# Performance work log

Measured on AMD Instinct MI355X. Metric: run time of the kernel, lower is better.

Reference implementation:

```python
import jax, jax.numpy as jnp
import numpy as np

INPUT_DIM = 512
EMBED_DIM = 512
N_HEAD = 8
HEAD_DIM = EMBED_DIM // N_HEAD


def setup_inputs() -> dict:
    key = jax.random.key(0)
    k0, k1, k2 = jax.random.split(key, 3)
    B, S = 2, 4096
    X = jax.random.normal(k0, (B, S, INPUT_DIM), dtype=jnp.float32)
    # xavier_uniform for Linear weights (torch weight shape [out, in])
    def xavier(k, out_f, in_f):
        bound = float(np.sqrt(6.0 / (in_f + out_f)))
        return jax.random.uniform(k, (out_f, in_f), jnp.float32, -bound, bound)
    W_qkv = xavier(k1, 3 * EMBED_DIM, INPUT_DIM)
    b_qkv = jnp.zeros((3 * EMBED_DIM,), jnp.float32)
    W_o = xavier(k2, EMBED_DIM, EMBED_DIM)
    b_o = jnp.zeros((EMBED_DIM,), jnp.float32)
    return {"X": X, "W_qkv": W_qkv, "b_qkv": b_qkv, "W_o": W_o, "b_o": b_o}


def reference(X, W_qkv, b_qkv, W_o, b_o):
    B, S, _ = X.shape
    # fused QKV projection: [B,S,3E]
    qkv = jnp.einsum("bsd,ed->bse", X, W_qkv) + b_qkv
    # [B,S,H,3*hd] -> [B,H,S,3*hd]
    qkv = qkv.reshape(B, S, N_HEAD, 3 * HEAD_DIM).transpose(0, 2, 1, 3)
    q, k, v = jnp.split(qkv, 3, axis=-1)
    scale = 1.0 / jnp.sqrt(jnp.asarray(HEAD_DIM, q.dtype))
    logits = jnp.einsum("bhqd,bhkd->bhqk", q, k) * scale  # [B,H,S,S]
    attn = jax.nn.softmax(logits, axis=-1)
    vals = jnp.einsum("bhqk,bhkd->bhqd", attn, v)
    vals = vals.transpose(0, 2, 1, 3).reshape(B, S, EMBED_DIM)
    out = jnp.einsum("bse,fe->bsf", vals, W_o) + b_o
    return out
```

## Files before the change

### kernel.cpp

```cpp
#include <hip/hip_runtime.h>

#define S_   4096
#define D_IN 512
#define E_   512
#define HD   64

typedef __attribute__((ext_vector_type(8))) short short8;
typedef __attribute__((ext_vector_type(16))) float f32x16;

#define MFMA32(a, b, c) __builtin_amdgcn_mfma_f32_32x32x16_bf16((a), (b), (c), 0, 0, 0)

__device__ __forceinline__ unsigned short f2bf(float f) {
  unsigned u = __builtin_bit_cast(unsigned, f);
  u = (u + 0x7FFFu + ((u >> 16) & 1u)) >> 16;
  return (unsigned short)u;
}

__device__ __forceinline__ unsigned cvt_pk_bf16(float lo, float hi) {
  unsigned r;
  asm("v_cvt_pk_bf16_f32 %0, %1, %2" : "=v"(r) : "v"(lo), "v"(hi));
  return r;
}

__device__ __forceinline__ f32x16 splat16(float x) {
  f32x16 v;
#pragma unroll
  for (int i = 0; i < 16; ++i) v[i] = x;
  return v;
}

__global__ __launch_bounds__(256) void cvt3(const float* __restrict__ X,
                                            const float* __restrict__ Wq,
                                            const float* __restrict__ Wo,
                                            unsigned short* __restrict__ Xb,
                                            unsigned short* __restrict__ Wqb,
                                            unsigned short* __restrict__ Wob) {
  int bid = blockIdx.x;
  const float* src;
  unsigned short* dst;
  int i;
  if (bid < 4096)      { src = X;  dst = Xb;  i = bid * 256 + threadIdx.x; }
  else if (bid < 4864) { src = Wq; dst = Wqb; i = (bid - 4096) * 256 + threadIdx.x; }
  else                 { src = Wo; dst = Wob; i = (bid - 4864) * 256 + threadIdx.x; }
  float4 v = reinterpret_cast<const float4*>(src)[i];
  ushort4 o;
  o.x = f2bf(v.x); o.y = f2bf(v.y); o.z = f2bf(v.z); o.w = f2bf(v.w);
  reinterpret_cast<ushort4*>(dst)[i] = o;
}

__global__ __launch_bounds__(256, 3) void qkv_proj(const unsigned short* __restrict__ Xb,
                                                   const unsigned short* __restrict__ Wb,
                                                   const float* __restrict__ bias,
                                                   unsigned short* __restrict__ Qb,
                                                   unsigned short* __restrict__ Kb,
                                                   unsigned short* __restrict__ Vt) {
  __shared__ unsigned short Al[128][72];
  __shared__ unsigned short Bl[128][72];
  const int tid = threadIdx.x;
  const int w = tid >> 6, l = tid & 63, h = l >> 5, r31 = l & 31;
  const int wm = w >> 1, wn = w & 1;
  const int m0 = blockIdx.x * 128, n0 = blockIdx.y * 128;
  const int sr = tid >> 1, sc = tid & 1;

  f32x16 a00 = {}, a01 = {}, a10 = {}, a11 = {};
  const unsigned short* ap = Xb + (size_t)(m0 + sr) * D_IN + sc * 32;
  const unsigned short* bp = Wb + (size_t)(n0 + sr) * D_IN + sc * 32;
  for (int k0 = 0; k0 < D_IN; k0 += 64) {
    int4 av0 = *reinterpret_cast<const int4*>(ap + k0);
    int4 av1 = *reinterpret_cast<const int4*>(ap + k0 + 8);
    int4 av2 = *reinterpret_cast<const int4*>(ap + k0 + 16);
    int4 av3 = *reinterpret_cast<const int4*>(ap + k0 + 24);
    int4 bv0 = *reinterpret_cast<const int4*>(bp + k0);
    int4 bv1 = *reinterpret_cast<const int4*>(bp + k0 + 8);
    int4 bv2 = *reinterpret_cast<const int4*>(bp + k0 + 16);
    int4 bv3 = *reinterpret_cast<const int4*>(bp + k0 + 24);
    __syncthreads();
    *reinterpret_cast<int4*>(&Al[sr][sc * 32])      = av0;
    *reinterpret_cast<int4*>(&Al[sr][sc * 32 + 8])  = av1;
    *reinterpret_cast<int4*>(&Al[sr][sc * 32 + 16]) = av2;
    *reinterpret_cast<int4*>(&Al[sr][sc * 32 + 24]) = av3;
    *reinterpret_cast<int4*>(&Bl[sr][sc * 32])      = bv0;
    *reinterpret_cast<int4*>(&Bl[sr][sc * 32 + 8])  = bv1;
    *reinterpret_cast<int4*>(&Bl[sr][sc * 32 + 16]) = bv2;
    *reinterpret_cast<int4*>(&Bl[sr][sc * 32 + 24]) = bv3;
    __syncthreads();
#pragma unroll
    for (int c = 0; c < 4; ++c) {
      short8 aA = *reinterpret_cast<const short8*>(&Al[wm * 64 + r31][c * 16 + h * 8]);
      short8 aB = *reinterpret_cast<const short8*>(&Al[wm * 64 + 32 + r31][c * 16 + h * 8]);
      short8 bA = *reinterpret_cast<const short8*>(&Bl[wn * 64 + r31][c * 16 + h * 8]);
      short8 bB = *reinterpret_cast<const short8*>(&Bl[wn * 64 + 32 + r31][c * 16 + h * 8]);
      a00 = MFMA32(aA, bA, a00);
      a01 = MFMA32(aA, bB, a01);
      a10 = MFMA32(aB, bA, a10);
      a11 = MFMA32(aB, bB, a11);
    }
  }
#pragma unroll
  for (int rb = 0; rb < 2; ++rb)
#pragma unroll
    for (int cb = 0; cb < 2; ++cb) {
      const f32x16 A = rb ? (cb ? a11 : a10) : (cb ? a01 : a00);
      int n = n0 + wn * 64 + cb * 32 + r31;
      int hh = n / 192;
      int j = n - hh * 192;
      int t3 = j >> 6;
      int d = j & 63;
      float bn = bias[n];
      int mbase0 = m0 + wm * 64 + rb * 32 + h * 4;
#pragma unroll
      for (int rq = 0; rq < 4; ++rq) {
        int mb = mbase0 + rq * 8;
        int bb = mb >> 12;
        int ssb = mb & 4095;
        int bhh = bb * 8 + hh;
        if (t3 == 0) {
#pragma unroll
          for (int i = 0; i < 4; ++i)
            Qb[((size_t)bhh * S_ + ssb + i) * HD + d] =
                f2bf((A[rq * 4 + i] + bn) * (0.125f * 1.44269504088896f));
        } else if (t3 == 1) {
#pragma unroll
          for (int i = 0; i < 4; ++i)
            Kb[((size_t)bhh * S_ + ssb + i) * HD + d] = f2bf(A[rq * 4 + i] + bn);
        } else {
          int sp = (ssb & ~12) | ((ssb & 8) >> 1) | ((ssb & 4) << 1);
          ushort4 o;
          o.x = f2bf(A[rq * 4 + 0] + bn);
          o.y = f2bf(A[rq * 4 + 1] + bn);
          o.z = f2bf(A[rq * 4 + 2] + bn);
          o.w = f2bf(A[rq * 4 + 3] + bn);
          *reinterpret_cast<ushort4*>(&Vt[((size_t)bhh * HD + d) * S_ + sp]) = o;
        }
      }
    }
}

__global__ __launch_bounds__(512, 4) void attn_fwd(const unsigned short* __restrict__ Qb,
                                                   const unsigned short* __restrict__ Kb,
                                                   const unsigned short* __restrict__ Vt,
                                                   unsigned short* __restrict__ vals) {
  __shared__ char smem[73728];
  const int tid = threadIdx.x;
  const int w = tid >> 6, l = tid & 63, h = l >> 5, r31 = l & 31;
  const int grp = w >> 2;
  const int wq = w & 3;
  const int bh = blockIdx.x >> 5;
  const int q0 = (blockIdx.x & 31) * 128;
  const int lt256 = tid & 255;
  const int sr = lt256 >> 2, sc = lt256 & 3;

  unsigned short (*Kl)[64][72] =
      reinterpret_cast<unsigned short(*)[64][72]>(smem + grp * 36864);
  unsigned short (*Vl)[64][72] =
      reinterpret_cast<unsigned short(*)[64][72]>(smem + grp * 36864 + 18432);

  const int qrow = q0 + wq * 32 + r31;
  const unsigned short* qp = Qb + ((size_t)bh * S_ + qrow) * HD + h * 8;
  short8 bq[4];
#pragma unroll
  for (int c = 0; c < 4; ++c)
    bq[c] = *reinterpret_cast<const short8*>(qp + c * 16);

  f32x16 po0 = {}, po1 = {};
  float lacc = 0.f;

  const int kvbase = grp * 2048;
  const unsigned short* kptr = Kb + ((size_t)bh * S_ + kvbase + sr) * HD + sc * 16;
  const unsigned short* vptr = Vt + ((size_t)bh * HD + sr) * S_ + kvbase + sc * 16;

  {
    int4 kA = *reinterpret_cast<const int4*>(kptr);
    int4 kB = *reinterpret_cast<const int4*>(kptr + 8);
    int4 vA = *reinterpret_cast<const int4*>(vptr);
    int4 vB = *reinterpret_cast<const int4*>(vptr + 8);
    *reinterpret_cast<int4*>(&Kl[0][sr][sc * 16])     = kA;
    *reinterpret_cast<int4*>(&Kl[0][sr][sc * 16 + 8]) = kB;
    *reinterpret_cast<int4*>(&Vl[0][sr][sc * 16])     = vA;
    *reinterpret_cast<int4*>(&Vl[0][sr][sc * 16 + 8]) = vB;
  }
  __syncthreads();

  for (int kt = 0; kt < 32; ++kt) {
    const int cur = kt & 1;
    int4 kA, kB, vA, vB;
    if (kt < 31) {
      const unsigned short* kp = kptr + (size_t)(kt + 1) * 64 * HD;
      const unsigned short* vp = vptr + (kt + 1) * 64;
      kA = *reinterpret_cast<const int4*>(kp);
      kB = *reinterpret_cast<const int4*>(kp + 8);
      vA = *reinterpret_cast<const int4*>(vp);
      vB = *reinterpret_cast<const int4*>(vp + 8);
    }

    f32x16 s0 = splat16(-16.f), s1 = splat16(-16.f);
#pragma unroll
    for (int c = 0; c < 4; ++c) {
      short8 k0 = *reinterpret_cast<const short8*>(&Kl[cur][r31][c * 16 + h * 8]);
      s0 = MFMA32(k0, bq[c], s0);
      short8 k1 = *reinterpret_cast<const short8*>(&Kl[cur][32 + r31][c * 16 + h * 8]);
      s1 = MFMA32(k1, bq[c], s1);
    }

#pragma unroll
    for (int i = 0; i < 16; ++i) {
      s0[i] = __builtin_amdgcn_exp2f(s0[i]);
      s1[i] = __builtin_amdgcn_exp2f(s1[i]);
    }
    float r0 = ((s0[0] + s0[1]) + (s0[2] + s0[3])) + ((s0[4] + s0[5]) + (s0[6] + s0[7]));
    float r1 = ((s0[8] + s0[9]) + (s0[10] + s0[11])) + ((s0[12] + s0[13]) + (s0[14] + s0[15]));
    float r2 = ((s1[0] + s1[1]) + (s1[2] + s1[3])) + ((s1[4] + s1[5]) + (s1[6] + s1[7]));
    float r3 = ((s1[8] + s1[9]) + (s1[10] + s1[11])) + ((s1[12] + s1[13]) + (s1[14] + s1[15]));
    lacc += (r0 + r1) + (r2 + r3);

#pragma unroll
    for (int c = 0; c < 4; ++c) {
      const f32x16 pp = (c < 2) ? s0 : s1;
      const int o8 = (c & 1) * 8;
      uint4 pk;
      pk.x = cvt_pk_bf16(pp[o8 + 0], pp[o8 + 1]);
      pk.y = cvt_pk_bf16(pp[o8 + 2], pp[o8 + 3]);
      pk.z = cvt_pk_bf16(pp[o8 + 4], pp[o8 + 5]);
      pk.w = cvt_pk_bf16(pp[o8 + 6], pp[o8 + 7]);
      short8 pf = __builtin_bit_cast(short8, pk);
      short8 v0 = *reinterpret_cast<const short8*>(&Vl[cur][r31][c * 16 + h * 8]);
      po0 = MFMA32(v0, pf, po0);
      short8 v1 = *reinterpret_cast<const short8*>(&Vl[cur][32 + r31][c * 16 + h * 8]);
      po1 = MFMA32(v1, pf, po1);
    }

    if (kt < 31) {
      *reinterpret_cast<int4*>(&Kl[cur ^ 1][sr][sc * 16])     = kA;
      *reinterpret_cast<int4*>(&Kl[cur ^ 1][sr][sc * 16 + 8]) = kB;
      *reinterpret_cast<int4*>(&Vl[cur ^ 1][sr][sc * 16])     = vA;
      *reinterpret_cast<int4*>(&Vl[cur ^ 1][sr][sc * 16 + 8]) = vB;
    }
    __syncthreads();
  }

  float ltp = lacc + __shfl_xor(lacc, 32);
  float* Ox = reinterpret_cast<float*>(smem);
  float* lx = reinterpret_cast<float*>(smem + 34816);
  const int qlocal = wq * 32 + r31;
  if (grp == 0) {
#pragma unroll
    for (int db = 0; db < 2; ++db) {
      const f32x16 P = db ? po1 : po0;
#pragma unroll
      for (int rq = 0; rq < 4; ++rq) {
        float4 st = {P[rq * 4 + 0], P[rq * 4 + 1], P[rq * 4 + 2], P[rq * 4 + 3]};
        *reinterpret_cast<float4*>(&Ox[qlocal * 68 + db * 32 + rq * 8 + h * 4]) = st;
      }
    }
    if (h == 0) lx[qlocal] = ltp;
  }
  __syncthreads();
  if (grp == 1) {
    float inv = 1.0f / (ltp + lx[qlocal]);
    const int b = bh >> 3, hd = bh & 7;
    unsigned short* op = vals + ((size_t)b * S_ + qrow) * E_ + hd * HD + h * 4;
#pragma unroll
    for (int db = 0; db < 2; ++db) {
      const f32x16 P = db ? po1 : po0;
#pragma unroll
      for (int rq = 0; rq < 4; ++rq) {
        float4 pv = *reinterpret_cast<const float4*>(&Ox[qlocal * 68 + db * 32 + rq * 8 + h * 4]);
        ushort4 o;
        o.x = f2bf((P[rq * 4 + 0] + pv.x) * inv);
        o.y = f2bf((P[rq * 4 + 1] + pv.y) * inv);
        o.z = f2bf((P[rq * 4 + 2] + pv.z) * inv);
        o.w = f2bf((P[rq * 4 + 3] + pv.w) * inv);
        *reinterpret_cast<ushort4*>(op + db * 32 + rq * 8) = o;
      }
    }
  }
}

__global__ __launch_bounds__(256, 3) void o_proj(const unsigned short* __restrict__ Ab,
                                                 const unsigned short* __restrict__ Wb,
                                                 const float* __restrict__ bias,
                                                 float* __restrict__ out) {
  __shared__ unsigned short Al[128][72];
  __shared__ unsigned short Bl[128][72];
  const int tid = threadIdx.x;
  const int w = tid >> 6, l = tid & 63, h = l >> 5, r31 = l & 31;
  const int wm = w >> 1, wn = w & 1;
  const int m0 = blockIdx.x * 128, n0 = blockIdx.y * 128;
  const int sr = tid >> 1, sc = tid & 1;

  f32x16 a00 = {}, a01 = {}, a10 = {}, a11 = {};
  const unsigned short* ap = Ab + (size_t)(m0 + sr) * E_ + sc * 32;
  const unsigned short* bp = Wb + (size_t)(n0 + sr) * E_ + sc * 32;
  for (int k0 = 0; k0 < E_; k0 += 64) {
    int4 av0 = *reinterpret_cast<const int4*>(ap + k0);
    int4 av1 = *reinterpret_cast<const int4*>(ap + k0 + 8);
    int4 av2 = *reinterpret_cast<const int4*>(ap + k0 + 16);
    int4 av3 = *reinterpret_cast<const int4*>(ap + k0 + 24);
    int4 bv0 = *reinterpret_cast<const int4*>(bp + k0);
    int4 bv1 = *reinterpret_cast<const int4*>(bp + k0 + 8);
    int4 bv2 = *reinterpret_cast<const int4*>(bp + k0 + 16);
    int4 bv3 = *reinterpret_cast<const int4*>(bp + k0 + 24);
    __syncthreads();
    *reinterpret_cast<int4*>(&Al[sr][sc * 32])      = av0;
    *reinterpret_cast<int4*>(&Al[sr][sc * 32 + 8])  = av1;
    *reinterpret_cast<int4*>(&Al[sr][sc * 32 + 16]) = av2;
    *reinterpret_cast<int4*>(&Al[sr][sc * 32 + 24]) = av3;
    *reinterpret_cast<int4*>(&Bl[sr][sc * 32])      = bv0;
    *reinterpret_cast<int4*>(&Bl[sr][sc * 32 + 8])  = bv1;
    *reinterpret_cast<int4*>(&Bl[sr][sc * 32 + 16]) = bv2;
    *reinterpret_cast<int4*>(&Bl[sr][sc * 32 + 24]) = bv3;
    __syncthreads();
#pragma unroll
    for (int c = 0; c < 4; ++c) {
      short8 aA = *reinterpret_cast<const short8*>(&Al[wm * 64 + r31][c * 16 + h * 8]);
      short8 aB = *reinterpret_cast<const short8*>(&Al[wm * 64 + 32 + r31][c * 16 + h * 8]);
      short8 bA = *reinterpret_cast<const short8*>(&Bl[wn * 64 + r31][c * 16 + h * 8]);
      short8 bB = *reinterpret_cast<const short8*>(&Bl[wn * 64 + 32 + r31][c * 16 + h * 8]);
      a00 = MFMA32(aA, bA, a00);
      a01 = MFMA32(aA, bB, a01);
      a10 = MFMA32(aB, bA, a10);
      a11 = MFMA32(aB, bB, a11);
    }
  }
#pragma unroll
  for (int rb = 0; rb < 2; ++rb)
#pragma unroll
    for (int cb = 0; cb < 2; ++cb) {
      const f32x16 A = rb ? (cb ? a11 : a10) : (cb ? a01 : a00);
      int n = n0 + wn * 64 + cb * 32 + r31;
      float bn = bias[n];
      int mbase0 = m0 + wm * 64 + rb * 32 + h * 4;
#pragma unroll
      for (int rq = 0; rq < 4; ++rq)
#pragma unroll
        for (int i = 0; i < 4; ++i)
          out[(size_t)(mbase0 + rq * 8 + i) * E_ + n] = A[rq * 4 + i] + bn;
    }
}

extern "C" void kernel_launch(void* const* d_in, const int* in_sizes, int n_in,
                              void* d_out, int out_size, void* d_ws, size_t ws_size,
                              hipStream_t stream) {
  const float* X    = (const float*)d_in[0];
  const float* Wqkv = (const float*)d_in[1];
  const float* bqkv = (const float*)d_in[2];
  const float* Wo   = (const float*)d_in[3];
  const float* bo   = (const float*)d_in[4];
  float* out = (float*)d_out;

  char* ws = (char*)d_ws;
  unsigned short* Xb   = (unsigned short*)(ws);
  unsigned short* Wqb  = (unsigned short*)(ws + 8388608);
  unsigned short* Wob  = (unsigned short*)(ws + 9961472);
  unsigned short* Qb   = (unsigned short*)(ws + 10485760);
  unsigned short* Kb   = (unsigned short*)(ws + 18874368);
  unsigned short* Vt   = (unsigned short*)(ws + 27262976);
  unsigned short* vals = (unsigned short*)(ws + 35651584);

  cvt3<<<5120, 256, 0, stream>>>(X, Wqkv, Wo, Xb, Wqb, Wob);
  qkv_proj<<<dim3(64, 12), 256, 0, stream>>>(Xb, Wqb, bqkv, Qb, Kb, Vt);
  attn_fwd<<<512, 512, 0, stream>>>(Qb, Kb, Vt, vals);
  o_proj<<<dim3(64, 4), 256, 0, stream>>>(vals, Wob, bo, out);
}
```

Before: 126.0 us.

## Load K/V tiles directly into LDS with global_load_lds and XOR swizzle

Replaces the register-staged global-to-LDS copy of K and V tiles with direct global_load_lds transfers of 16 bytes per lane. The padded 72-column LDS layout becomes an unpadded 64-column layout with an XOR swizzle on 16-byte chunks to avoid bank conflicts, which shrinks shared memory from 72KB to 64KB. This removes the VGPRs that held prefetched data and the separate ds_write step, at the cost of relying on the async LDS-load ordering and the barrier being enough to make the data visible.

```diff
diff --git a/kernel.cpp b/kernel.cpp
--- a/kernel.cpp
+++ b/kernel.cpp
@@ -27,6 +27,12 @@
 #pragma unroll
   for (int i = 0; i < 16; ++i) v[i] = x;
   return v;
+}
+
+__device__ __forceinline__ void gload_lds16(const void* g, void* l) {
+  __builtin_amdgcn_global_load_lds(
+      (const __attribute__((address_space(1))) unsigned int*)g,
+      (__attribute__((address_space(3))) unsigned int*)l, 16, 0, 0);
 }
 
 __global__ __launch_bounds__(256) void cvt3(const float* __restrict__ X,
@@ -140,20 +146,13 @@
                                                    const unsigned short* __restrict__ Kb,
                                                    const unsigned short* __restrict__ Vt,
                                                    unsigned short* __restrict__ vals) {
-  __shared__ char smem[73728];
+  __shared__ char smem[65536];
   const int tid = threadIdx.x;
   const int w = tid >> 6, l = tid & 63, h = l >> 5, r31 = l & 31;
   const int grp = w >> 2;
   const int wq = w & 3;
   const int bh = blockIdx.x >> 5;
   const int q0 = (blockIdx.x & 31) * 128;
-  const int lt256 = tid & 255;
-  const int sr = lt256 >> 2, sc = lt256 & 3;
-
-  unsigned short (*Kl)[64][72] =
-      reinterpret_cast<unsigned short(*)[64][72]>(smem + grp * 36864);
-  unsigned short (*Vl)[64][72] =
-      reinterpret_cast<unsigned short(*)[64][72]>(smem + grp * 36864 + 18432);
 
   const int qrow = q0 + wq * 32 + r31;
   const unsigned short* qp = Qb + ((size_t)bh * S_ + qrow) * HD + h * 8;
@@ -166,39 +165,49 @@
   float lacc = 0.f;
 
   const int kvbase = grp * 2048;
-  const unsigned short* kptr = Kb + ((size_t)bh * S_ + kvbase + sr) * HD + sc * 16;
-  const unsigned short* vptr = Vt + ((size_t)bh * HD + sr) * S_ + kvbase + sc * 16;
-
-  {
-    int4 kA = *reinterpret_cast<const int4*>(kptr);
-    int4 kB = *reinterpret_cast<const int4*>(kptr + 8);
-    int4 vA = *reinterpret_cast<const int4*>(vptr);
-    int4 vB = *reinterpret_cast<const int4*>(vptr + 8);
-    *reinterpret_cast<int4*>(&Kl[0][sr][sc * 16])     = kA;
-    *reinterpret_cast<int4*>(&Kl[0][sr][sc * 16 + 8]) = kB;
-    *reinterpret_cast<int4*>(&Vl[0][sr][sc * 16])     = vA;
-    *reinterpret_cast<int4*>(&Vl[0][sr][sc * 16 + 8]) = vB;
-  }
+
+  const int lrow = l >> 3;
+  const int lchunk = (l & 7) ^ lrow;
+  const unsigned short* pK = Kb + ((size_t)bh * S_ + kvbase + wq * 16 + lrow) * HD + lchunk * 8;
+  const unsigned short* pV = Vt + ((size_t)bh * HD + wq * 16 + lrow) * S_ + kvbase + lchunk * 8;
+
+  char* gbase = smem + grp * 32768;
+  char* dK = gbase + wq * 2048;
+  char* dV = gbase + 16384 + wq * 2048;
+
+  const int sx = r31 & 7;
+  int ko[4];
+#pragma unroll
+  for (int c = 0; c < 4; ++c)
+    ko[c] = r31 * 128 + (((2 * c + h) ^ sx) * 16);
+
+  gload_lds16(pK,            dK);
+  gload_lds16(pK + 8 * HD,   dK + 1024);
+  gload_lds16(pV,            dV);
+  gload_lds16(pV + 8 * S_,   dV + 1024);
   __syncthreads();
 
   for (int kt = 0; kt < 32; ++kt) {
     const int cur = kt & 1;
-    int4 kA, kB, vA, vB;
     if (kt < 31) {
-      const unsigned short* kp = kptr + (size_t)(kt + 1) * 64 * HD;
-      const unsigned short* vp = vptr + (kt + 1) * 64;
-      kA = *reinterpret_cast<const int4*>(kp);
-      kB = *reinterpret_cast<const int4*>(kp + 8);
-      vA = *reinterpret_cast<const int4*>(vp);
-      vB = *reinterpret_cast<const int4*>(vp + 8);
-    }
+      const unsigned short* sK = pK + (size_t)(kt + 1) * 64 * HD;
+      const unsigned short* sV = pV + (kt + 1) * 64;
+      char* nK = dK + (cur ^ 1) * 8192;
+      char* nV = dV + (cur ^ 1) * 8192;
+      gload_lds16(sK,          nK);
+      gload_lds16(sK + 8 * HD, nK + 1024);
+      gload_lds16(sV,          nV);
+      gload_lds16(sV + 8 * S_, nV + 1024);
+    }
+    const char* kb = gbase + cur * 8192;
+    const char* vb = gbase + 16384 + cur * 8192;
 
     f32x16 s0 = splat16(-16.f), s1 = splat16(-16.f);
 #pragma unroll
     for (int c = 0; c < 4; ++c) {
-      short8 k0 = *reinterpret_cast<const short8*>(&Kl[cur][r31][c * 16 + h * 8]);
+      short8 k0 = *reinterpret_cast<const short8*>(kb + ko[c]);
       s0 = MFMA32(k0, bq[c], s0);
-      short8 k1 = *reinterpret_cast<const short8*>(&Kl[cur][32 + r31][c * 16 + h * 8]);
+      short8 k1 = *reinterpret_cast<const short8*>(kb + ko[c] + 4096);
       s1 = MFMA32(k1, bq[c], s1);
     }
 
@@ -223,18 +232,12 @@
       pk.z = cvt_pk_bf16(pp[o8 + 4], pp[o8 + 5]);
       pk.w = cvt_pk_bf16(pp[o8 + 6], pp[o8 + 7]);
       short8 pf = __builtin_bit_cast(short8, pk);
-      short8 v0 = *reinterpret_cast<const short8*>(&Vl[cur][r31][c * 16 + h * 8]);
+      short8 v0 = *reinterpret_cast<const short8*>(vb + ko[c]);
       po0 = MFMA32(v0, pf, po0);
-      short8 v1 = *reinterpret_cast<const short8*>(&Vl[cur][32 + r31][c * 16 + h * 8]);
+      short8 v1 = *reinterpret_cast<const short8*>(vb + ko[c] + 4096);
       po1 = MFMA32(v1, pf, po1);
     }
 
-    if (kt < 31) {
-      *reinterpret_cast<int4*>(&Kl[cur ^ 1][sr][sc * 16])     = kA;
-      *reinterpret_cast<int4*>(&Kl[cur ^ 1][sr][sc * 16 + 8]) = kB;
-      *reinterpret_cast<int4*>(&Vl[cur ^ 1][sr][sc * 16])     = vA;
-      *reinterpret_cast<int4*>(&Vl[cur ^ 1][sr][sc * 16 + 8]) = vB;
-    }
     __syncthreads();
   }
 
```

Result: slower. 152.2 us (+20.7%).
